# Performance work log

Hardware: AMD Instinct MI355X
Metric: run time of the kernel (lower is better)

## Reference

```python
import jax, jax.numpy as jnp
import numpy as np

C = 1.0          # curvature args.c
ALPHA = 3.0      # self.alpha
MIN = 1e-15      # min_norm clamp (HGCN PoincareBall)
PROJ_EPS = 4e-3  # fp32 boundary eps (HGCN)


def _norm(x):
    return jnp.maximum(jnp.linalg.norm(x, axis=-1, keepdims=True), MIN)


def artanh(x):
    # clamp for fp32 stability (HGCN clamps to 1 - 1e-15; 1e-7 is the fp32 analogue)
    return jnp.arctanh(jnp.clip(x, -1.0 + 1e-7, 1.0 - 1e-7))


def proj(x, c):
    n = _norm(x)
    maxn = (1.0 - PROJ_EPS) / jnp.sqrt(c)
    return jnp.where(n > maxn, x / n * maxn, x)


def expmap0(u, c):
    sc = jnp.sqrt(c)
    n = _norm(u)
    return jnp.tanh(sc * n) * u / (sc * n)


def logmap0(p, c):
    sc = jnp.sqrt(c)
    n = _norm(p)
    return artanh(sc * n) * p / (sc * n)


def mobius_add(x, y, c):
    x2 = jnp.sum(x * x, axis=-1, keepdims=True)
    y2 = jnp.sum(y * y, axis=-1, keepdims=True)
    xy = jnp.sum(x * y, axis=-1, keepdims=True)
    num = (1.0 + 2.0 * c * xy + c * y2) * x + (1.0 - c * x2) * y
    den = 1.0 + 2.0 * c * xy + c * c * x2 * y2
    return num / jnp.maximum(den, MIN)


def mobius_matvec(m, x, c):
    sc = jnp.sqrt(c)
    xn = _norm(x)
    mx = x @ m.T                      # [..., out]
    mxn = _norm(mx)
    res = jnp.tanh(mxn / xn * artanh(sc * xn)) * mx / (mxn * sc)
    zero_rows = jnp.all(mx == 0.0, axis=-1, keepdims=True)
    return jnp.where(zero_rows, 0.0, res)


def hyp_linear(x, W, b, c):
    # dropout on weights is identity in eval mode
    mv = proj(mobius_matvec(W, x, c), c)
    hb = proj(expmap0(b[None, :], c), c)  # proj_tan0 is identity on Poincare ball
    return proj(mobius_add(mv, hb, c), c)


def setup_inputs() -> dict:
    key = jax.random.key(0)
    N, D, F = 8192, 128, 128
    ks = jax.random.split(key, 8)
    gain = np.sqrt(2.0 / (D + D)) * np.sqrt(2.0)  # xavier-like scale
    return {
        "idx": jnp.arange(N, dtype=jnp.int32),
        "dist_metrix": jnp.zeros((1,), dtype=jnp.float32),
        "x": jax.random.normal(ks[0], (N, F), dtype=jnp.float32),
        "emb1": jax.random.normal(ks[1], (N, D), dtype=jnp.float32),
        "emb2": jax.random.normal(ks[2], (N, D), dtype=jnp.float32),
        "W1": jax.random.normal(ks[3], (D, D), dtype=jnp.float32) * gain,
        "b1": jax.random.normal(ks[4], (D,), dtype=jnp.float32) * 0.01,
        "W2": jax.random.normal(ks[5], (D, D), dtype=jnp.float32) * gain,
        "b2": jax.random.normal(ks[6], (D,), dtype=jnp.float32) * 0.01,
    }


def reference(idx, dist_metrix, x, emb1, emb2, W1, b1, W2, b2):
    # node embeddings lifted to the Poincare ball (proj_tan0 is identity)
    nv1 = proj(expmap0(emb1[idx], C), C)
    nv2 = proj(expmap0(emb2[idx], C), C)
    nv1 = hyp_linear(nv1, W1, b1, C)
    nv2 = hyp_linear(nv2, W2, b2, C)
    # adjacency construction: a1 = nv2 @ nv1^T (mobius), a2 = nv1 @ nv2^T (mobius)
    a1 = mobius_matvec(nv1, nv2, C)   # [N, N]
    a2 = mobius_matvec(nv2, nv1, C)   # [N, N]
    a = mobius_add(a1, -a2, C)
    adj = jax.nn.relu(jnp.tanh(ALPHA * a))
    n = adj.shape[0]
    adj = adj + 1e-4 * jnp.eye(n, dtype=adj.dtype)
    # row-normalize (scipy round-trip in original == row-sum divide, inf -> 0)
    rs = jnp.sum(adj, axis=1, keepdims=True)
    adj = adj * jnp.where(rs == 0.0, 0.0, 1.0 / rs)
    # propagate features
    xt = logmap0(x, C)                       # [N, F]
    out = mobius_matvec(xt.T, adj, C)        # adj @ xt -> [N, F]
    out = logmap0(out, C)
    return out
```

## Files before the change

kernel.cpp:

```cpp
#include <hip/hip_runtime.h>
#include <hip/hip_bf16.h>


typedef __attribute__((ext_vector_type(8))) short short8;
typedef __attribute__((ext_vector_type(4))) float f32x4;

#define MAXN 0.996f

__device__ __forceinline__ float artanh_clip(float x) {
    x = fminf(x, 1.0f - 1e-7f);
    x = fmaxf(x, -1.0f + 1e-7f);
    return 0.5f * logf((1.0f + x) / (1.0f - x));
}

__device__ __forceinline__ float red8(float v) {
    v += __shfl_xor(v, 1);
    v += __shfl_xor(v, 2);
    v += __shfl_xor(v, 4);
    return v;
}

__device__ __forceinline__ float red64(float v) {
#pragma unroll
    for (int m = 1; m < 64; m <<= 1) v += __shfl_xor(v, m);
    return v;
}

__device__ __forceinline__ unsigned short f2bf(float f) {
    __hip_bfloat16 h = __float2bfloat16(f);
    return *reinterpret_cast<unsigned short*>(&h);
}

__device__ __forceinline__ float bf2f(unsigned short u) {
    __hip_bfloat16 h;
    *reinterpret_cast<unsigned short*>(&h) = u;
    return __bfloat162float(h);
}

__global__ __launch_bounds__(256) void prep_kernel(
    const int* __restrict__ idx, const float* __restrict__ x,
    const float* __restrict__ emb1, const float* __restrict__ emb2,
    const float* __restrict__ W1, const float* __restrict__ W2,
    const float* __restrict__ b1, const float* __restrict__ b2,
    unsigned short* __restrict__ nv1b, unsigned short* __restrict__ nv2b,
    unsigned short* __restrict__ xtT,
    float* __restrict__ xn1, float* __restrict__ xn2) {
    const int which = blockIdx.y;
    const int tid = threadIdx.x;
    const int rblk = blockIdx.x * 32;

    if (which == 2) {
        __shared__ float xv[32 * 132];
        const int r = tid >> 3, s = tid & 7;
        float ev[16];
        float p2 = 0.f;
#pragma unroll
        for (int kk = 0; kk < 16; ++kk) {
            float e = x[(rblk + r) * 128 + s + kk * 8];
            ev[kk] = e;
            p2 += e * e;
        }
        const float n = fmaxf(sqrtf(red8(p2)), 1e-15f);
        const float scl = artanh_clip(n) / n;
#pragma unroll
        for (int kk = 0; kk < 16; ++kk) xv[r * 132 + s + kk * 8] = ev[kk] * scl;
        __syncthreads();
        const int k = tid >> 1, h = tid & 1;
        short8 o0, o1;
#pragma unroll
        for (int j = 0; j < 8; ++j) o0[j] = (short)f2bf(xv[(h * 16 + j) * 132 + k]);
#pragma unroll
        for (int j = 0; j < 8; ++j) o1[j] = (short)f2bf(xv[(h * 16 + 8 + j) * 132 + k]);
        *reinterpret_cast<short8*>(&xtT[k * 8192 + rblk + h * 16]) = o0;
        *reinterpret_cast<short8*>(&xtT[k * 8192 + rblk + h * 16 + 8]) = o1;
        return;
    }

    __shared__ __align__(16) float uL[32 * 132];
    __shared__ float mxL[32 * 132];
    __shared__ float xnL[32];
    __shared__ float hbL[128];
    __shared__ float s2s[4];

    const float* emb = which ? emb2 : emb1;
    const float* W = which ? W2 : W1;
    const float* b = which ? b2 : b1;
    unsigned short* nvb = which ? nv2b : nv1b;
    float* xno = which ? xn2 : xn1;

    float bv = (tid < 128) ? b[tid] : 0.f;
    float ssq = red64(bv * bv);
    if ((tid & 63) == 0) s2s[tid >> 6] = ssq;
    __syncthreads();
    const float bn = fmaxf(sqrtf(s2s[0] + s2s[1]), 1e-15f);
    const float bth = tanhf(bn);
    const float bnu = fmaxf(bth, 1e-15f);
    const float bps = (bnu > MAXN) ? (MAXN / bnu) : 1.0f;
    if (tid < 128) hbL[tid] = bv * (bth / bn) * bps;
    const float hbn = fminf(bnu, MAXN);
    const float y2 = hbn * hbn;

    const int r = tid >> 3, s = tid & 7;
    const int row = rblk + r;
    const int src = idx[row];
    float ev[16];
    float p2 = 0.f;
#pragma unroll
    for (int kk = 0; kk < 16; ++kk) {
        float e = emb[src * 128 + s + kk * 8];
        ev[kk] = e;
        p2 += e * e;
    }
    float n2 = red8(p2);
    float n = fmaxf(sqrtf(n2), 1e-15f);
    float th = tanhf(n);
    float nu = fmaxf(th, 1e-15f);
    float ps = (nu > MAXN) ? (MAXN / nu) : 1.0f;
    float sc0 = (th / n) * ps;
#pragma unroll
    for (int kk = 0; kk < 16; ++kk) uL[r * 132 + s + kk * 8] = ev[kk] * sc0;
    if (s == 0) xnL[r] = fmaxf(nu * ps, 1e-15f);
    __syncthreads();

    const int o = tid & 127, rb = tid >> 7;
    float mxv[16];
#pragma unroll
    for (int rr = 0; rr < 16; ++rr) mxv[rr] = 0.f;
    for (int k4 = 0; k4 < 128; k4 += 4) {
        const float4 wv = *reinterpret_cast<const float4*>(&W[o * 128 + k4]);
#pragma unroll
        for (int rr = 0; rr < 16; ++rr) {
            const float4 uv = *reinterpret_cast<const float4*>(&uL[(rb + rr * 2) * 132 + k4]);
            mxv[rr] += uv.x * wv.x + uv.y * wv.y + uv.z * wv.z + uv.w * wv.w;
        }
    }
#pragma unroll
    for (int rr = 0; rr < 16; ++rr) mxL[(rb + rr * 2) * 132 + o] = mxv[rr];
    __syncthreads();

    float mx[16];
    float m2 = 0.f;
#pragma unroll
    for (int kk = 0; kk < 16; ++kk) {
        mx[kk] = mxL[r * 132 + s + kk * 8];
        m2 += mx[kk] * mx[kk];
    }
    float mxn = fmaxf(sqrtf(red8(m2)), 1e-15f);
    float xnv = xnL[r];
    float tt = tanhf(mxn / xnv * artanh_clip(xnv));
    float nres = fmaxf(tt, 1e-15f);
    float ps2 = (nres > MAXN) ? (MAXN / nres) : 1.0f;
    float s2 = (tt / mxn) * ps2;
    float mvn = nres * ps2;
    float x2 = mvn * mvn;
    float xyp = 0.f;
    float mv[16];
#pragma unroll
    for (int kk = 0; kk < 16; ++kk) {
        mv[kk] = mx[kk] * s2;
        xyp += mv[kk] * hbL[s + kk * 8];
    }
    float xy = red8(xyp);
    float cA = 1.f + 2.f * xy + y2;
    float cB = 1.f - x2;
    float rden = 1.f / fmaxf(1.f + 2.f * xy + x2 * y2, 1e-15f);
    float r2v[16];
    float q2 = 0.f;
#pragma unroll
    for (int kk = 0; kk < 16; ++kk) {
        float v = (cA * mv[kk] + cB * hbL[s + kk * 8]) * rden;
        r2v[kk] = v;
        q2 += v * v;
    }
    float nr2 = fmaxf(sqrtf(red8(q2)), 1e-15f);
    float ps3 = (nr2 > MAXN) ? (MAXN / nr2) : 1.0f;
#pragma unroll
    for (int kk = 0; kk < 16; ++kk) nvb[row * 128 + s + kk * 8] = f2bf(r2v[kk] * ps3);
    if (s == 0) xno[row] = fmaxf((nr2 > MAXN) ? MAXN : nr2, 1e-15f);
}

__global__ __launch_bounds__(256) void gram_kernel(const unsigned short* __restrict__ nv1b,
                                                   const unsigned short* __restrict__ nv2b,
                                                   float* __restrict__ G) {
    __shared__ float Ab[64 * 33], Bb[64 * 33];
    const int tile = blockIdx.x, mat = blockIdx.y, kc = blockIdx.z;
    const int ta = (tile & 3) * 32, tb = (tile >> 2) * 32;
    const unsigned short* Am = (mat == 1) ? nv2b : nv1b;
    const unsigned short* Bm = (mat == 0) ? nv1b : nv2b;
    const int tid = threadIdx.x;
    const int oa = tid & 31, obb = (tid >> 5) * 4;
    float acc[4] = {0.f, 0.f, 0.f, 0.f};
    for (int sc = 0; sc < 16; ++sc) {
        const int r0 = kc * 1024 + sc * 64;
        for (int i0 = tid; i0 < 2048; i0 += 256) {
            int rr = i0 >> 5, cc = i0 & 31;
            Ab[rr * 33 + cc] = bf2f(Am[(r0 + rr) * 128 + ta + cc]);
            Bb[rr * 33 + cc] = bf2f(Bm[(r0 + rr) * 128 + tb + cc]);
        }
        __syncthreads();
#pragma unroll 4
        for (int rr = 0; rr < 64; ++rr) {
            float av = Ab[rr * 33 + oa];
#pragma unroll
            for (int i = 0; i < 4; ++i) acc[i] += av * Bb[rr * 33 + obb + i];
        }
        __syncthreads();
    }
#pragma unroll
    for (int i = 0; i < 4; ++i)
        atomicAdd(&G[mat * 16384 + (ta + oa) * 128 + tb + obb + i], acc[i]);
}

__global__ __launch_bounds__(256) void rowcoef_kernel(
    const float* __restrict__ G, const float* __restrict__ xn1, const float* __restrict__ xn2,
    const unsigned short* __restrict__ nv1b, const unsigned short* __restrict__ nv2b,
    float* __restrict__ P, float* __restrict__ Q) {
    __shared__ __align__(16) float v1L[32 * 132];
    __shared__ __align__(16) float v2L[32 * 132];
    __shared__ float tL[32 * 132];
    __shared__ float RCX[3][32];
    const int tid = threadIdx.x;
    const int rblk = blockIdx.x * 32;
    for (int i = tid; i < 4096; i += 256) {
        int r = i >> 7, c = i & 127;
        v1L[r * 132 + c] = bf2f(nv1b[(rblk + r) * 128 + c]);
        v2L[r * 132 + c] = bf2f(nv2b[(rblk + r) * 128 + c]);
    }
    __syncthreads();
    const int o = tid & 127, rb = tid >> 7;
    const int rA = tid >> 3, sA = tid & 7;
    for (int mat = 0; mat < 3; ++mat) {
        const float* vR = (mat == 0) ? v2L : v1L;
        const float* vL = (mat == 1) ? v1L : v2L;
        const float* Gm = G + mat * 16384;
        float tv[16];
#pragma unroll
        for (int rr = 0; rr < 16; ++rr) tv[rr] = 0.f;
        for (int k4 = 0; k4 < 128; k4 += 4) {
            const float4 gv = *reinterpret_cast<const float4*>(&Gm[o * 128 + k4]);
#pragma unroll
            for (int rr = 0; rr < 16; ++rr) {
                const float4 uv = *reinterpret_cast<const float4*>(&vR[(rb + rr * 2) * 132 + k4]);
                tv[rr] += uv.x * gv.x + uv.y * gv.y + uv.z * gv.z + uv.w * gv.w;
            }
        }
        __syncthreads();
#pragma unroll
        for (int rr = 0; rr < 16; ++rr) {
            int rw = rb + rr * 2;
            tL[rw * 132 + o] = vL[rw * 132 + o] * tv[rr];
        }
        __syncthreads();
        float p = 0.f;
#pragma unroll
        for (int kk = 0; kk < 16; ++kk) p += tL[rA * 132 + sA + kk * 8];
        p = red8(p);
        if (sA == 0) RCX[mat][rA] = p;
    }
    __syncthreads();
    if (tid < 32) {
        const int row = rblk + tid;
        const float R = RCX[0][tid], Cc = RCX[1][tid], X = RCX[2][tid];
        const float xn1v = xn1[row], xn2v = xn2[row];
        const float mxn1 = fmaxf(sqrtf(fmaxf(R, 0.f)), 1e-15f);
        const float t1 = tanhf(mxn1 / xn2v * artanh_clip(xn2v));
        const float f1 = t1 / mxn1;
        const float mxn2 = fmaxf(sqrtf(fmaxf(Cc, 0.f)), 1e-15f);
        const float t2 = tanhf(mxn2 / xn1v * artanh_clip(xn1v));
        const float f2 = t2 / mxn2;
        const float x2 = f1 * f1 * R, y2 = f2 * f2 * Cc;
        const float xy = -f1 * f2 * X;
        const float rden = 1.f / fmaxf(1.f + 2.f * xy + x2 * y2, 1e-15f);
        P[row] = (1.f + 2.f * xy + y2) * f1 * rden;
        Q[row] = -(1.f - x2) * f2 * rden;
    }
}

__global__ __launch_bounds__(512, 2) void fused_kernel(
    const unsigned short* __restrict__ nv1b, const unsigned short* __restrict__ nv2b,
    const unsigned short* __restrict__ xtT,
    const float* __restrict__ P, const float* __restrict__ Q,
    float* __restrict__ U, float* __restrict__ rs, float* __restrict__ qs) {
    __shared__ float S1[32 * 132];
    __shared__ __align__(16) unsigned short adjb[32 * 136];
    __shared__ float PL[32], QL[32];
    __shared__ int s2flag;

    const int tid = threadIdx.x;
    const int w = tid >> 6, l = tid & 63;
    const int b = blockIdx.x;
    const int xcd = b & 7, slot = b >> 3;
    const int js = xcd >> 1;
    const int iblk = ((xcd & 1) * 128 + slot) * 32;
    const int jb0 = js * 16;

    if (tid == 0) s2flag = 0;
    if (tid < 32) {
        PL[tid] = P[iblk + tid];
        QL[tid] = Q[iblk + tid];
    }
    __syncthreads();
    if (tid < 32 && fabsf(QL[tid]) > 1e-6f) atomicOr(&s2flag, 1);
    __syncthreads();
    const bool needS2 = (s2flag != 0);

    short8 areg[2][4];
#pragma unroll
    for (int tr = 0; tr < 2; ++tr)
#pragma unroll
        for (int kk = 0; kk < 4; ++kk)
            areg[tr][kk] = *reinterpret_cast<const short8*>(
                &nv2b[(iblk + tr * 16 + (l & 15)) * 128 + kk * 32 + (l >> 4) * 8]);

    const f32x4 zero4 = {0.f, 0.f, 0.f, 0.f};
    f32x4 accU[2];
    accU[0] = zero4;
    accU[1] = zero4;
    float rsA[4] = {0.f, 0.f, 0.f, 0.f};
    float qA[4] = {0.f, 0.f, 0.f, 0.f};

    auto computeS1 = [&](int jb) {
        const int jblk = jb * 128;
        f32x4 acc0 = zero4, acc1 = zero4;
#pragma unroll
        for (int kk = 0; kk < 4; ++kk) {
            short8 bfr = *reinterpret_cast<const short8*>(
                &nv1b[(jblk + w * 16 + (l & 15)) * 128 + kk * 32 + (l >> 4) * 8]);
            acc0 = __builtin_amdgcn_mfma_f32_16x16x32_bf16(areg[0][kk], bfr, acc0, 0, 0, 0);
            acc1 = __builtin_amdgcn_mfma_f32_16x16x32_bf16(areg[1][kk], bfr, acc1, 0, 0, 0);
        }
#pragma unroll
        for (int v = 0; v < 4; ++v) {
            S1[((l >> 4) * 4 + v) * 132 + w * 16 + (l & 15)] = acc0[v];
            S1[(16 + (l >> 4) * 4 + v) * 132 + w * 16 + (l & 15)] = acc1[v];
        }
    };

    auto s2merge = [&](int jb) {
        const int jblk = jb * 128;
        f32x4 a20 = zero4, a21 = zero4;
#pragma unroll
        for (int kk = 0; kk < 4; ++kk) {
            short8 a2 = *reinterpret_cast<const short8*>(
                &nv2b[(jblk + w * 16 + (l & 15)) * 128 + kk * 32 + (l >> 4) * 8]);
            short8 b20 = *reinterpret_cast<const short8*>(
                &nv1b[(iblk + (l & 15)) * 128 + kk * 32 + (l >> 4) * 8]);
            short8 b21 = *reinterpret_cast<const short8*>(
                &nv1b[(iblk + 16 + (l & 15)) * 128 + kk * 32 + (l >> 4) * 8]);
            a20 = __builtin_amdgcn_mfma_f32_16x16x32_bf16(a2, b20, a20, 0, 0, 0);
            a21 = __builtin_amdgcn_mfma_f32_16x16x32_bf16(a2, b21, a21, 0, 0, 0);
        }
        const int jloc = w * 16 + (l >> 4) * 4;
        const int i0 = l & 15;
#pragma unroll
        for (int v = 0; v < 4; ++v) {
            S1[i0 * 132 + jloc + v] = PL[i0] * S1[i0 * 132 + jloc + v] + QL[i0] * a20[v];
            S1[(i0 + 16) * 132 + jloc + v] =
                PL[i0 + 16] * S1[(i0 + 16) * 132 + jloc + v] + QL[i0 + 16] * a21[v];
        }
    };

    computeS1(jb0);
    for (int jb = jb0; jb < jb0 + 16; ++jb) {
        const int jblk = jb * 128;
        __syncthreads();
        if (needS2) {
            s2merge(jb);
            __syncthreads();
        }
        auto adjLoop = [&](bool dodiag) {
#pragma unroll
            for (int k = 0; k < 4; ++k) {
                const int r = w + 8 * k;
                const float Pv = PL[r];
#pragma unroll
                for (int h = 0; h < 2; ++h) {
                    const int c = l + 64 * h;
                    float sv = S1[r * 132 + c];
                    float a = needS2 ? sv : Pv * sv;
                    float e = __builtin_amdgcn_exp2f(a * 8.65617025f);
                    float t = 1.0f - 2.0f * __builtin_amdgcn_rcpf(e + 1.0f);
                    float ad = fmaxf(t, 0.0f);
                    if (dodiag && (iblk + r == jblk + c)) ad += 1e-4f;
                    rsA[k] += ad;
                    qA[k] += ad * ad;
                    adjb[r * 136 + c] = f2bf(ad);
                }
            }
        };
        if ((unsigned)(iblk - jblk) < 128u) adjLoop(true); else adjLoop(false);
        __syncthreads();
#pragma unroll
        for (int kk = 0; kk < 4; ++kk) {
            short8 bfr = *reinterpret_cast<const short8*>(
                &xtT[(w * 16 + (l & 15)) * 8192 + jblk + kk * 32 + (l >> 4) * 8]);
#pragma unroll
            for (int tr = 0; tr < 2; ++tr) {
                short8 a = *reinterpret_cast<const short8*>(
                    &adjb[(tr * 16 + (l & 15)) * 136 + kk * 32 + (l >> 4) * 8]);
                accU[tr] = __builtin_amdgcn_mfma_f32_16x16x32_bf16(a, bfr, accU[tr], 0, 0, 0);
            }
        }
        if (jb + 1 < jb0 + 16) computeS1(jb + 1);
    }

#pragma unroll
    for (int tr = 0; tr < 2; ++tr)
#pragma unroll
        for (int v = 0; v < 4; ++v)
            atomicAdd(&U[(iblk + tr * 16 + (l >> 4) * 4 + v) * 128 + w * 16 + (l & 15)],
                      accU[tr][v]);
#pragma unroll
    for (int k = 0; k < 4; ++k) {
        float rsv = red64(rsA[k]);
        float qv = red64(qA[k]);
        if (l == 0) {
            atomicAdd(&rs[iblk + w + 8 * k], rsv);
            atomicAdd(&qs[iblk + w + 8 * k], qv);
        }
    }
}

__global__ __launch_bounds__(256) void finalize_kernel(
    const float* __restrict__ U, const float* __restrict__ rs,
    const float* __restrict__ qs, float* __restrict__ out) {
    const int tid = threadIdx.x;
    const int row = blockIdx.x * 4 + (tid >> 6);
    const int l = tid & 63;
    const float u0 = U[row * 128 + l], u1 = U[row * 128 + 64 + l];
    const float rsv = rs[row];
    const float wv = (rsv == 0.f) ? 0.f : 1.f / rsv;
    const float m0 = u0 * wv, m1 = u1 * wv;
    const float mxn = fmaxf(sqrtf(red64(m0 * m0 + m1 * m1)), 1e-15f);
    const float xn = fmaxf(sqrtf(fmaxf(qs[row], 0.f)) * wv, 1e-15f);
    const float tt = tanhf(mxn / xn * artanh_clip(xn));
    const float nres = fmaxf(tt, 1e-15f);
    const float lsc = (tt / mxn) * (artanh_clip(nres) / nres);
    out[row * 128 + l] = m0 * lsc;
    out[row * 128 + 64 + l] = m1 * lsc;
}

extern "C" void kernel_launch(void* const* d_in, const int* in_sizes, int n_in,
                              void* d_out, int out_size, void* d_ws, size_t ws_size,
                              hipStream_t stream) {
    const int* idx = (const int*)d_in[0];
    const float* x = (const float*)d_in[2];
    const float* emb1 = (const float*)d_in[3];
    const float* emb2 = (const float*)d_in[4];
    const float* W1 = (const float*)d_in[5];
    const float* b1 = (const float*)d_in[6];
    const float* W2 = (const float*)d_in[7];
    const float* b2 = (const float*)d_in[8];
    float* out = (float*)d_out;
    char* ws = (char*)d_ws;

    unsigned short* nv1b = (unsigned short*)(ws + 0x000000);
    unsigned short* nv2b = (unsigned short*)(ws + 0x200000);
    unsigned short* xtT = (unsigned short*)(ws + 0x400000);
    float* G = (float*)(ws + 0x600000);
    float* xn1 = (float*)(ws + 0x630000);
    float* xn2 = (float*)(ws + 0x638000);
    float* P = (float*)(ws + 0x640000);
    float* Q = (float*)(ws + 0x648000);
    float* rs = (float*)(ws + 0x650000);
    float* qs = (float*)(ws + 0x658000);
    float* U = out;

    hipMemsetAsync(G, 0, 3 * 128 * 128 * sizeof(float), stream);
    hipMemsetAsync(rs, 0, 8192 * sizeof(float), stream);
    hipMemsetAsync(qs, 0, 8192 * sizeof(float), stream);
    hipMemsetAsync(U, 0, 8192 * 128 * sizeof(float), stream);
    prep_kernel<<<dim3(256, 3), 256, 0, stream>>>(idx, x, emb1, emb2, W1, W2, b1, b2,
                                                  nv1b, nv2b, xtT, xn1, xn2);
    gram_kernel<<<dim3(16, 3, 8), 256, 0, stream>>>(nv1b, nv2b, G);
    rowcoef_kernel<<<256, 256, 0, stream>>>(G, xn1, xn2, nv1b, nv2b, P, Q);
    fused_kernel<<<1024, 512, 0, stream>>>(nv1b, nv2b, xtT, P, Q, U, rs, qs);
    finalize_kernel<<<2048, 256, 0, stream>>>(U, rs, qs, out);
    (void)in_sizes; (void)n_in; (void)out_size; (void)ws_size; (void)d_in;
}
```

Measured before the change: 344.8 us.

## Keep adjacency tiles in registers and fuse finalize into fused kernel

Restructures the fused kernel so each block owns 32 full rows and loops over all columns itself, with each wave processing interleaved 32-column slices. The adjacency values are computed straight from MFMA accumulators and packed in registers as the A operand for the propagation MFMA, which removes the shared-memory S1/adjb round trips and the per-step block barriers. Row sums and the output matrix are reduced in shared memory, and the finalize/logmap step runs inside the same kernel, so the global atomics, three memsets and the separate finalize launch are gone. In exchange the grid drops from 1024 to 256 blocks, which may leave many CUs idle, and register pressure rises from the 16 accumulator tiles per wave.

```diff
diff --git a/kernel.cpp b/kernel.cpp
--- a/kernel.cpp
+++ b/kernel.cpp
@@ -276,168 +276,168 @@
     }
 }
 
-__global__ __launch_bounds__(512, 2) void fused_kernel(
+__global__ __launch_bounds__(512) void fused_kernel(
     const unsigned short* __restrict__ nv1b, const unsigned short* __restrict__ nv2b,
     const unsigned short* __restrict__ xtT,
     const float* __restrict__ P, const float* __restrict__ Q,
-    float* __restrict__ U, float* __restrict__ rs, float* __restrict__ qs) {
-    __shared__ float S1[32 * 132];
-    __shared__ __align__(16) unsigned short adjb[32 * 136];
-    __shared__ float PL[32], QL[32];
-    __shared__ int s2flag;
+    float* __restrict__ out) {
+    __shared__ float UL[32 * 132];
+    __shared__ float rsL[32], qL[32];
 
     const int tid = threadIdx.x;
     const int w = tid >> 6, l = tid & 63;
-    const int b = blockIdx.x;
-    const int xcd = b & 7, slot = b >> 3;
-    const int js = xcd >> 1;
-    const int iblk = ((xcd & 1) * 128 + slot) * 32;
-    const int jb0 = js * 16;
-
-    if (tid == 0) s2flag = 0;
-    if (tid < 32) {
-        PL[tid] = P[iblk + tid];
-        QL[tid] = Q[iblk + tid];
-    }
-    __syncthreads();
-    if (tid < 32 && fabsf(QL[tid]) > 1e-6f) atomicOr(&s2flag, 1);
-    __syncthreads();
-    const bool needS2 = (s2flag != 0);
-
-    short8 areg[2][4];
-#pragma unroll
-    for (int tr = 0; tr < 2; ++tr)
-#pragma unroll
-        for (int kk = 0; kk < 4; ++kk)
-            areg[tr][kk] = *reinterpret_cast<const short8*>(
-                &nv2b[(iblk + tr * 16 + (l & 15)) * 128 + kk * 32 + (l >> 4) * 8]);
-
-    const f32x4 zero4 = {0.f, 0.f, 0.f, 0.f};
-    f32x4 accU[2];
-    accU[0] = zero4;
-    accU[1] = zero4;
-    float rsA[4] = {0.f, 0.f, 0.f, 0.f};
-    float qA[4] = {0.f, 0.f, 0.f, 0.f};
-
-    auto computeS1 = [&](int jb) {
-        const int jblk = jb * 128;
-        f32x4 acc0 = zero4, acc1 = zero4;
+    const int g = l >> 4, c = l & 15;
+    const int i0 = blockIdx.x * 32;
+
+    for (int i = tid; i < 32 * 132; i += 512) UL[i] = 0.f;
+    if (tid < 32) { rsL[tid] = 0.f; qL[tid] = 0.f; }
+    __syncthreads();
+
+    const float Pv0 = P[i0 + c], Pv1 = P[i0 + 16 + c];
+    const float Qv0 = Q[i0 + c], Qv1 = Q[i0 + 16 + c];
+    const bool needS2 = __any((fabsf(Qv0) > 1e-6f) || (fabsf(Qv1) > 1e-6f)) != 0;
+
+    short8 Bn0[4], Bn1[4];
+#pragma unroll
+    for (int kk = 0; kk < 4; ++kk) {
+        Bn0[kk] = *reinterpret_cast<const short8*>(nv2b + (i0 + c) * 128 + kk * 32 + g * 8);
+        Bn1[kk] = *reinterpret_cast<const short8*>(nv2b + (i0 + 16 + c) * 128 + kk * 32 + g * 8);
+    }
+
+    const f32x4 z4 = {0.f, 0.f, 0.f, 0.f};
+    f32x4 accU0[8], accU1[8];
+#pragma unroll
+    for (int ft = 0; ft < 8; ++ft) { accU0[ft] = z4; accU1[ft] = z4; }
+    float rs0 = 0.f, rs1 = 0.f, q0 = 0.f, q1 = 0.f;
+
+    const int aoff = (8 * (c >> 2) + (c & 3)) * 128 + g * 8;
+    const int sdiag = i0 >> 5;
+    const int tdiag = ((sdiag & 7) == w) ? (sdiag >> 3) : -1;
+    const size_t xoff = (size_t)c * 8192 + g * 8;
+
+    auto elem = [&](float s, float s2v, float Pv, float Qv, int jglob, int iglob,
+                    bool dd, float& rsa, float& qa) -> float {
+        float a = Pv * s;
+        if (needS2) a = fmaf(Qv, s2v, a);
+        float e = __builtin_amdgcn_exp2f(a * 8.65617025f);
+        float t = 1.0f - 2.0f * __builtin_amdgcn_rcpf(e + 1.0f);
+        float ad = fmaxf(t, 0.0f);
+        if (dd && (jglob == iglob)) ad += 1e-4f;
+        rsa += ad;
+        qa = fmaf(ad, ad, qa);
+        return ad;
+    };
+    auto pack8 = [](const float* ad) -> short8 {
+        union { unsigned u[4]; short8 s; } r;
+#pragma unroll
+        for (int k = 0; k < 4; ++k)
+            r.u[k] = (unsigned)f2bf(ad[2 * k]) | ((unsigned)f2bf(ad[2 * k + 1]) << 16);
+        return r.s;
+    };
+
+    auto doStep = [&](int jb, bool dd) __attribute__((always_inline)) {
+        const unsigned short* pa = nv1b + (size_t)jb * 128;
+        short8 A0[4], A1[4];
 #pragma unroll
         for (int kk = 0; kk < 4; ++kk) {
-            short8 bfr = *reinterpret_cast<const short8*>(
-                &nv1b[(jblk + w * 16 + (l & 15)) * 128 + kk * 32 + (l >> 4) * 8]);
-            acc0 = __builtin_amdgcn_mfma_f32_16x16x32_bf16(areg[0][kk], bfr, acc0, 0, 0, 0);
-            acc1 = __builtin_amdgcn_mfma_f32_16x16x32_bf16(areg[1][kk], bfr, acc1, 0, 0, 0);
-        }
+            A0[kk] = *reinterpret_cast<const short8*>(pa + aoff + kk * 32);
+            A1[kk] = *reinterpret_cast<const short8*>(pa + aoff + 512 + kk * 32);
+        }
+        f32x4 s00 = z4, s10 = z4, s01 = z4, s11 = z4;
+#pragma unroll
+        for (int kk = 0; kk < 4; ++kk) {
+            s00 = __builtin_amdgcn_mfma_f32_16x16x32_bf16(A0[kk], Bn0[kk], s00, 0, 0, 0);
+            s10 = __builtin_amdgcn_mfma_f32_16x16x32_bf16(A1[kk], Bn0[kk], s10, 0, 0, 0);
+            s01 = __builtin_amdgcn_mfma_f32_16x16x32_bf16(A0[kk], Bn1[kk], s01, 0, 0, 0);
+            s11 = __builtin_amdgcn_mfma_f32_16x16x32_bf16(A1[kk], Bn1[kk], s11, 0, 0, 0);
+        }
+        f32x4 r00 = z4, r10 = z4, r01 = z4, r11 = z4;
+        if (needS2) {
+            const unsigned short* pa2 = nv2b + (size_t)jb * 128;
+            short8 C0[4], C1[4], D0[4], D1[4];
+#pragma unroll
+            for (int kk = 0; kk < 4; ++kk) {
+                C0[kk] = *reinterpret_cast<const short8*>(pa2 + aoff + kk * 32);
+                C1[kk] = *reinterpret_cast<const short8*>(pa2 + aoff + 512 + kk * 32);
+                D0[kk] = *reinterpret_cast<const short8*>(nv1b + (i0 + c) * 128 + kk * 32 + g * 8);
+                D1[kk] = *reinterpret_cast<const short8*>(nv1b + (i0 + 16 + c) * 128 + kk * 32 + g * 8);
+            }
+#pragma unroll
+            for (int kk = 0; kk < 4; ++kk) {
+                r00 = __builtin_amdgcn_mfma_f32_16x16x32_bf16(C0[kk], D0[kk], r00, 0, 0, 0);
+                r10 = __builtin_amdgcn_mfma_f32_16x16x32_bf16(C1[kk], D0[kk], r10, 0, 0, 0);
+                r01 = __builtin_amdgcn_mfma_f32_16x16x32_bf16(C0[kk], D1[kk], r01, 0, 0, 0);
+                r11 = __builtin_amdgcn_mfma_f32_16x16x32_bf16(C1[kk], D1[kk], r11, 0, 0, 0);
+            }
+        }
+        float ad0[8], ad1[8];
+        const int jg = jb + 8 * g;
+        const int ig0 = i0 + c, ig1 = i0 + 16 + c;
 #pragma unroll
         for (int v = 0; v < 4; ++v) {
-            S1[((l >> 4) * 4 + v) * 132 + w * 16 + (l & 15)] = acc0[v];
-            S1[(16 + (l >> 4) * 4 + v) * 132 + w * 16 + (l & 15)] = acc1[v];
+            ad0[v]     = elem(s00[v], r00[v], Pv0, Qv0, jg + v,     ig0, dd, rs0, q0);
+            ad0[4 + v] = elem(s10[v], r10[v], Pv0, Qv0, jg + 4 + v, ig0, dd, rs0, q0);
+            ad1[v]     = elem(s01[v], r01[v], Pv1, Qv1, jg + v,     ig1, dd, rs1, q1);
+            ad1[4 + v] = elem(s11[v], r11[v], Pv1, Qv1, jg + 4 + v, ig1, dd, rs1, q1);
+        }
+        const short8 af0 = pack8(ad0);
+        const short8 af1 = pack8(ad1);
+#pragma unroll
+        for (int ft = 0; ft < 8; ++ft) {
+            short8 xb = *reinterpret_cast<const short8*>(xtT + (size_t)ft * 16 * 8192 + xoff + jb);
+            accU0[ft] = __builtin_amdgcn_mfma_f32_16x16x32_bf16(af0, xb, accU0[ft], 0, 0, 0);
+            accU1[ft] = __builtin_amdgcn_mfma_f32_16x16x32_bf16(af1, xb, accU1[ft], 0, 0, 0);
         }
     };
 
-    auto s2merge = [&](int jb) {
-        const int jblk = jb * 128;
-        f32x4 a20 = zero4, a21 = zero4;
-#pragma unroll
-        for (int kk = 0; kk < 4; ++kk) {
-            short8 a2 = *reinterpret_cast<const short8*>(
-                &nv2b[(jblk + w * 16 + (l & 15)) * 128 + kk * 32 + (l >> 4) * 8]);
-            short8 b20 = *reinterpret_cast<const short8*>(
-                &nv1b[(iblk + (l & 15)) * 128 + kk * 32 + (l >> 4) * 8]);
-            short8 b21 = *reinterpret_cast<const short8*>(
-                &nv1b[(iblk + 16 + (l & 15)) * 128 + kk * 32 + (l >> 4) * 8]);
-            a20 = __builtin_amdgcn_mfma_f32_16x16x32_bf16(a2, b20, a20, 0, 0, 0);
-            a21 = __builtin_amdgcn_mfma_f32_16x16x32_bf16(a2, b21, a21, 0, 0, 0);
-        }
-        const int jloc = w * 16 + (l >> 4) * 4;
-        const int i0 = l & 15;
+    for (int t = 0; t < 32; ++t) {
+        const int jb = (w + 8 * t) * 32;
+        if (t == tdiag) doStep(jb, true);
+        else doStep(jb, false);
+    }
+
+    rs0 += __shfl_xor(rs0, 16); rs0 += __shfl_xor(rs0, 32);
+    rs1 += __shfl_xor(rs1, 16); rs1 += __shfl_xor(rs1, 32);
+    q0 += __shfl_xor(q0, 16);   q0 += __shfl_xor(q0, 32);
+    q1 += __shfl_xor(q1, 16);   q1 += __shfl_xor(q1, 32);
+    if (l < 16) {
+        atomicAdd(&rsL[c], rs0);
+        atomicAdd(&qL[c], q0);
+        atomicAdd(&rsL[16 + c], rs1);
+        atomicAdd(&qL[16 + c], q1);
+    }
+#pragma unroll
+    for (int ft = 0; ft < 8; ++ft)
 #pragma unroll
         for (int v = 0; v < 4; ++v) {
-            S1[i0 * 132 + jloc + v] = PL[i0] * S1[i0 * 132 + jloc + v] + QL[i0] * a20[v];
-            S1[(i0 + 16) * 132 + jloc + v] =
-                PL[i0 + 16] * S1[(i0 + 16) * 132 + jloc + v] + QL[i0 + 16] * a21[v];
-        }
-    };
-
-    computeS1(jb0);
-    for (int jb = jb0; jb < jb0 + 16; ++jb) {
-        const int jblk = jb * 128;
-        __syncthreads();
-        if (needS2) {
-            s2merge(jb);
-            __syncthreads();
-        }
-        auto adjLoop = [&](bool dodiag) {
-#pragma unroll
-            for (int k = 0; k < 4; ++k) {
-                const int r = w + 8 * k;
-                const float Pv = PL[r];
-#pragma unroll
-                for (int h = 0; h < 2; ++h) {
-                    const int c = l + 64 * h;
-                    float sv = S1[r * 132 + c];
-                    float a = needS2 ? sv : Pv * sv;
-                    float e = __builtin_amdgcn_exp2f(a * 8.65617025f);
-                    float t = 1.0f - 2.0f * __builtin_amdgcn_rcpf(e + 1.0f);
-                    float ad = fmaxf(t, 0.0f);
-                    if (dodiag && (iblk + r == jblk + c)) ad += 1e-4f;
-                    rsA[k] += ad;
-                    qA[k] += ad * ad;
-                    adjb[r * 136 + c] = f2bf(ad);
-                }
-            }
-        };
-        if ((unsigned)(iblk - jblk) < 128u) adjLoop(true); else adjLoop(false);
-        __syncthreads();
-#pragma unroll
-        for (int kk = 0; kk < 4; ++kk) {
-            short8 bfr = *reinterpret_cast<const short8*>(
-                &xtT[(w * 16 + (l & 15)) * 8192 + jblk + kk * 32 + (l >> 4) * 8]);
-#pragma unroll
-            for (int tr = 0; tr < 2; ++tr) {
-                short8 a = *reinterpret_cast<const short8*>(
-                    &adjb[(tr * 16 + (l & 15)) * 136 + kk * 32 + (l >> 4) * 8]);
-                accU[tr] = __builtin_amdgcn_mfma_f32_16x16x32_bf16(a, bfr, accU[tr], 0, 0, 0);
-            }
-        }
-        if (jb + 1 < jb0 + 16) computeS1(jb + 1);
-    }
-
-#pragma unroll
-    for (int tr = 0; tr < 2; ++tr)
-#pragma unroll
-        for (int v = 0; v < 4; ++v)
-            atomicAdd(&U[(iblk + tr * 16 + (l >> 4) * 4 + v) * 128 + w * 16 + (l & 15)],
-                      accU[tr][v]);
-#pragma unroll
-    for (int k = 0; k < 4; ++k) {
-        float rsv = red64(rsA[k]);
-        float qv = red64(qA[k]);
-        if (l == 0) {
-            atomicAdd(&rs[iblk + w + 8 * k], rsv);
-            atomicAdd(&qs[iblk + w + 8 * k], qv);
-        }
-    }
-}
-
-__global__ __launch_bounds__(256) void finalize_kernel(
-    const float* __restrict__ U, const float* __restrict__ rs,
-    const float* __restrict__ qs, float* __restrict__ out) {
-    const int tid = threadIdx.x;
-    const int row = blockIdx.x * 4 + (tid >> 6);
-    const int l = tid & 63;
-    const float u0 = U[row * 128 + l], u1 = U[row * 128 + 64 + l];
-    const float rsv = rs[row];
+            atomicAdd(&UL[(4 * g + v) * 132 + ft * 16 + c], accU0[ft][v]);
+            atomicAdd(&UL[(16 + 4 * g + v) * 132 + ft * 16 + c], accU1[ft][v]);
+        }
+    __syncthreads();
+
+    const int r = tid >> 4, cc = tid & 15;
+    const float rsv = rsL[r];
     const float wv = (rsv == 0.f) ? 0.f : 1.f / rsv;
-    const float m0 = u0 * wv, m1 = u1 * wv;
-    const float mxn = fmaxf(sqrtf(red64(m0 * m0 + m1 * m1)), 1e-15f);
-    const float xn = fmaxf(sqrtf(fmaxf(qs[row], 0.f)) * wv, 1e-15f);
+    float m[8];
+    float m2 = 0.f;
+#pragma unroll
+    for (int e = 0; e < 8; ++e) {
+        m[e] = UL[r * 132 + cc * 8 + e] * wv;
+        m2 = fmaf(m[e], m[e], m2);
+    }
+    m2 += __shfl_xor(m2, 1);
+    m2 += __shfl_xor(m2, 2);
+    m2 += __shfl_xor(m2, 4);
+    m2 += __shfl_xor(m2, 8);
+    const float mxn = fmaxf(sqrtf(m2), 1e-15f);
+    const float xn = fmaxf(sqrtf(fmaxf(qL[r], 0.f)) * wv, 1e-15f);
     const float tt = tanhf(mxn / xn * artanh_clip(xn));
     const float nres = fmaxf(tt, 1e-15f);
     const float lsc = (tt / mxn) * (artanh_clip(nres) / nres);
-    out[row * 128 + l] = m0 * lsc;
-    out[row * 128 + 64 + l] = m1 * lsc;
+    float4 o0 = {m[0] * lsc, m[1] * lsc, m[2] * lsc, m[3] * lsc};
+    float4 o1 = {m[4] * lsc, m[5] * lsc, m[6] * lsc, m[7] * lsc};
+    *reinterpret_cast<float4*>(out + (i0 + r) * 128 + cc * 8) = o0;
+    *reinterpret_cast<float4*>(out + (i0 + r) * 128 + cc * 8 + 4) = o1;
 }
 
 extern "C" void kernel_launch(void* const* d_in, const int* in_sizes, int n_in,
@@ -462,19 +462,12 @@
     float* xn2 = (float*)(ws + 0x638000);
     float* P = (float*)(ws + 0x640000);
     float* Q = (float*)(ws + 0x648000);
-    float* rs = (float*)(ws + 0x650000);
-    float* qs = (float*)(ws + 0x658000);
-    float* U = out;
 
     hipMemsetAsync(G, 0, 3 * 128 * 128 * sizeof(float), stream);
-    hipMemsetAsync(rs, 0, 8192 * sizeof(float), stream);
-    hipMemsetAsync(qs, 0, 8192 * sizeof(float), stream);
-    hipMemsetAsync(U, 0, 8192 * 128 * sizeof(float), stream);
     prep_kernel<<<dim3(256, 3), 256, 0, stream>>>(idx, x, emb1, emb2, W1, W2, b1, b2,
                                                   nv1b, nv2b, xtT, xn1, xn2);
     gram_kernel<<<dim3(16, 3, 8), 256, 0, stream>>>(nv1b, nv2b, G);
     rowcoef_kernel<<<256, 256, 0, stream>>>(G, xn1, xn2, nv1b, nv2b, P, Q);
-    fused_kernel<<<1024, 512, 0, stream>>>(nv1b, nv2b, xtT, P, Q, U, rs, qs);
-    finalize_kernel<<<2048, 256, 0, stream>>>(U, rs, qs, out);
+    fused_kernel<<<256, 512, 0, stream>>>(nv1b, nv2b, xtT, P, Q, out);
     (void)in_sizes; (void)n_in; (void)out_size; (void)ws_size; (void)d_in;
 }
```

After: 350.5 us. About the same (+1.6%).
